# Optimization experiments

Measured on AMD Instinct MI355X. Metric: run time of the kernel, lower is better.

The kernel has to match this reference:

```python
import jax, jax.numpy as jnp
import numpy as np

E, C = 50000, 128  # edges, out_channels (heads=1 so H*C == C)
EPS = 1e-5

def _ln(x, g, b):
    m = x.mean(-1, keepdims=True)
    v = x.var(-1, keepdims=True)
    return (x - m) / jnp.sqrt(v + EPS) * g + b

def _mlp(x, W1, b1, W2, b2):
    return jax.nn.silu(x @ W1 + b1) @ W2 + b2

def setup_inputs() -> dict:
    key = jax.random.key(0)
    ks = jax.random.split(key, 32)
    s = 0.02
    d = {}
    d['edge'] = jax.random.normal(ks[0], (E, C), jnp.float32)
    d['edge_nei_len'] = jax.random.normal(ks[1], (E, 3, C), jnp.float32)
    d['edge_nei_angle'] = jax.random.normal(ks[2], (E, 3, C), jnp.float32)
    # lin_query / lin_key / lin_value (C -> H*C == C)
    d['Wq'] = jax.random.normal(ks[3], (C, C), jnp.float32) * s
    d['bq'] = jnp.zeros((C,), jnp.float32)
    d['Wk'] = jax.random.normal(ks[4], (C, C), jnp.float32) * s
    d['bk'] = jnp.zeros((C,), jnp.float32)
    d['Wv'] = jax.random.normal(ks[5], (C, C), jnp.float32) * s
    d['bv'] = jnp.zeros((C,), jnp.float32)
    # lin_key_e1/e2/e3 and lin_value_e1/e2/e3 stacked along first axis (3 lattice dirs)
    d['Wke'] = jax.random.normal(ks[6], (3, C, C), jnp.float32) * s
    d['bke'] = jnp.zeros((3, C), jnp.float32)
    d['Wve'] = jax.random.normal(ks[7], (3, C, C), jnp.float32) * s
    d['bve'] = jnp.zeros((3, C), jnp.float32)
    # lin_edge (no bias)
    d['We'] = jax.random.normal(ks[8], (C, C), jnp.float32) * s
    # lin_concate
    d['Wc'] = jax.random.normal(ks[9], (C, C), jnp.float32) * s
    d['bc'] = jnp.zeros((C,), jnp.float32)
    # key_update MLP: 3C -> C -> C
    d['Wk1'] = jax.random.normal(ks[10], (3 * C, C), jnp.float32) * s
    d['bk1'] = jnp.zeros((C,), jnp.float32)
    d['Wk2'] = jax.random.normal(ks[11], (C, C), jnp.float32) * s
    d['bk2'] = jnp.zeros((C,), jnp.float32)
    # lin_msg_update MLP: 3C -> C -> C
    d['Wm1'] = jax.random.normal(ks[12], (3 * C, C), jnp.float32) * s
    d['bm1'] = jnp.zeros((C,), jnp.float32)
    d['Wm2'] = jax.random.normal(ks[13], (C, C), jnp.float32) * s
    d['bm2'] = jnp.zeros((C,), jnp.float32)
    # LayerNorms
    d['g_att'] = jnp.ones((C,), jnp.float32)
    d['b_att'] = jnp.zeros((C,), jnp.float32)
    d['g_bn'] = jnp.ones((C,), jnp.float32)
    d['b_bn'] = jnp.zeros((C,), jnp.float32)
    return d

def reference(edge, edge_nei_len, edge_nei_angle,
              Wq, bq, Wk, bk, Wv, bv,
              Wke, bke, Wve, bve, We, Wc, bc,
              Wk1, bk1, Wk2, bk2, Wm1, bm1, Wm2, bm2,
              g_att, b_att, g_bn, b_bn):
    # per-edge projections, broadcast over the 3 lattice directions (repeat in torch)
    q = (edge @ Wq + bq)[:, None, :]           # [E,1,C]
    kx = (edge @ Wk + bk)[:, None, :]          # [E,1,C]
    vx = (edge @ Wv + bv)[:, None, :]          # [E,1,C]
    kx3 = jnp.broadcast_to(kx, (edge.shape[0], 3, kx.shape[-1]))
    vx3 = jnp.broadcast_to(vx, (edge.shape[0], 3, vx.shape[-1]))
    # per-direction projections of lattice embedding (lin_key_e1..3 / lin_value_e1..3)
    ky = jnp.einsum('eti,tio->eto', edge_nei_len, Wke) + bke   # [E,3,C]
    vy = jnp.einsum('eti,tio->eto', edge_nei_len, Wve) + bve   # [E,3,C]
    exy = edge_nei_angle @ We                                   # [E,3,C]
    # key_update MLP and attention score
    k = _mlp(jnp.concatenate([kx3, ky, exy], axis=-1), Wk1, bk1, Wk2, bk2)  # [E,3,C]
    alpha = q * k / jnp.sqrt(jnp.float32(k.shape[-1]))
    # message MLP, sigmoid gate on LayerNorm'd alpha
    msg = _mlp(jnp.concatenate([vx3, vy, exy], axis=-1), Wm1, bm1, Wm2, bm2)
    out = msg * jax.nn.sigmoid(_ln(alpha, g_att, b_att))
    out = out @ Wc + bc        # lin_concate (H*C -> C)
    out = out.sum(axis=1)      # sum over 3 directions -> [E,C]
    return jax.nn.softplus(edge + _ln(out, g_bn, b_bn))
```

## Files before the change

kernel.cpp:

```cpp
#include <hip/hip_runtime.h>

#define E_TOTAL 50000
#define NTILES  3125

#define OFF_WSB 458752ull
#define OFF_Q   524288ull
#define OFF_EK  (OFF_Q  + 12800000ull)
#define OFF_EM  (OFF_EK + 12800000ull)
#define OFF_SK  (OFF_EM + 12800000ull)
#define OFF_SM  (OFF_SK + 38400000ull)
#define WS_NEED (OFF_SM + 38400000ull)

typedef float f4  __attribute__((ext_vector_type(4)));
typedef short s8v __attribute__((ext_vector_type(8)));
typedef short s4v __attribute__((ext_vector_type(4)));

typedef __attribute__((address_space(3))) unsigned lds_u32;
typedef __attribute__((address_space(1))) const unsigned g_u32;

__device__ __forceinline__ short f2bf(float x){
  unsigned u = __builtin_bit_cast(unsigned, x);
  u += 0x7fffu + ((u >> 16) & 1u);
  return (short)(u >> 16);
}
__device__ __forceinline__ float bf2f(short s){
  unsigned u = ((unsigned)(unsigned short)s) << 16;
  return __builtin_bit_cast(float, u);
}
__device__ __forceinline__ float sigm(float x){ return 1.f/(1.f + __expf(-x)); }

__device__ __forceinline__ s8v load_bfrag(const float* p){
  f4 a = *(const f4*)p;
  f4 b = *(const f4*)(p + 4);
  s8v r;
  r[0]=f2bf(a[0]); r[1]=f2bf(a[1]); r[2]=f2bf(a[2]); r[3]=f2bf(a[3]);
  r[4]=f2bf(b[0]); r[5]=f2bf(b[1]); r[6]=f2bf(b[2]); r[7]=f2bf(b[3]);
  return r;
}

__device__ __forceinline__ void mm8l(f4* acc, const s8v* B, const s8v* A, int lane){
  #pragma unroll
  for (int mb = 0; mb < 8; ++mb){
    #pragma unroll
    for (int kk = 0; kk < 4; ++kk){
      s8v af = A[(mb*4 + kk)*64 + lane];
      acc[mb] = __builtin_amdgcn_mfma_f32_16x16x32_bf16(af, B[kk], acc[mb], 0, 0, 0);
    }
  }
}

__device__ __forceinline__ void mm8f(f4* acc, const s8v* B, const s8v* A, int lane){
  #pragma unroll
  for (int mb = 0; mb < 8; mb += 2){
    #pragma unroll
    for (int m2 = 0; m2 < 2; ++m2){
      #pragma unroll
      for (int kk = 0; kk < 4; ++kk){
        s8v af = A[((mb+m2)*4 + kk)*64 + lane];
        acc[mb+m2] = __builtin_amdgcn_mfma_f32_16x16x32_bf16(af, B[kk], acc[mb+m2], 0, 0, 0);
      }
    }
    __builtin_amdgcn_sched_barrier(0);
  }
}

__device__ __forceinline__ void stage_mat(const short* __restrict__ src,
                                          short* dst, int wid, int lane){
  #pragma unroll
  for (int j = 0; j < 8; ++j){
    const short* gsrc = src + j*2048 + wid*512 + lane*8;
    short* ldst = dst + j*2048 + wid*512;
    __builtin_amdgcn_global_load_lds((g_u32*)(const void*)gsrc, (lds_u32*)(void*)ldst, 16, 0, 0);
  }
}

__device__ __forceinline__ s8v pack_pair(const f4& a0, const f4& a1){
  s8v o;
  #pragma unroll
  for (int p = 0; p < 4; ++p){ o[p] = f2bf(a0[p]); o[4+p] = f2bf(a1[p]); }
  return o;
}

__global__ __launch_bounds__(256) void pack_weights(
    const float* __restrict__ Wq, const float* __restrict__ Wk, const float* __restrict__ Wv,
    const float* __restrict__ Wke, const float* __restrict__ Wve, const float* __restrict__ We,
    const float* __restrict__ Wc, const float* __restrict__ Wk1, const float* __restrict__ Wk2,
    const float* __restrict__ Wm1, const float* __restrict__ Wm2,
    short* __restrict__ wsm)
{
  int mi   = blockIdx.x >> 6;
  int elem = ((blockIdx.x & 63) << 8) + threadIdx.x;
  int p  = elem & 7;
  int l  = (elem >> 3) & 63;
  int kk = (elem >> 9) & 3;
  int mb = elem >> 11;
  int gg = l >> 4;
  int m  = mb*16 + (l & 15);
  bool dlay = (mi == 5) || (mi == 6) || (mi == 7);
  int k = dlay ? (kk*32 + ((p < 4) ? (gg*4 + p) : (16 + gg*4 + (p - 4))))
               : (kk*32 + gg*8 + p);

  const float* X = nullptr; const float* Y = nullptr; const float* W = nullptr;
  switch (mi){
    case 0: W = Wq; break;
    case 1: X = Wk; Y = Wk1;            break;
    case 2: X = Wv; Y = Wm1;            break;
    case 3: X = We; Y = Wk1 + 256*128;  break;
    case 4: X = We; Y = Wm1 + 256*128;  break;
    case 5: W = Wk2; break;
    case 6: W = Wm2; break;
    case 7: W = Wc;  break;
    default:
      if (mi < 11){ X = Wke + (mi-8)*16384;  Y = Wk1 + 128*128; }
      else        { X = Wve + (mi-11)*16384; Y = Wm1 + 128*128; }
  }
  float v;
  if (W){
    v = W[k*128 + m];
  } else {
    v = 0.f;
    for (int j = 0; j < 128; ++j) v += X[k*128 + j] * Y[j*128 + m];
  }
  wsm[(size_t)mi*16384 + elem] = f2bf(v);
}

__global__ __launch_bounds__(128) void make_biases(
    const float* __restrict__ bk,  const float* __restrict__ bke, const float* __restrict__ bk1,
    const float* __restrict__ bv,  const float* __restrict__ bve, const float* __restrict__ bm1,
    const float* __restrict__ Wk1, const float* __restrict__ Wm1,
    float* __restrict__ wsb)
{
  int b = blockIdx.x;
  int t = b % 3;
  bool isM = b >= 3;
  int o = threadIdx.x;
  const float* W  = isM ? Wm1 : Wk1;
  const float* b0 = isM ? bv  : bk;
  const float* be = (isM ? bve : bke) + t*128;
  const float* b1 = isM ? bm1 : bk1;
  float v = b1[o];
  for (int j = 0; j < 128; ++j)
    v += b0[j]*W[j*128 + o] + be[j]*W[(128 + j)*128 + o];
  wsb[b*128 + o] = v;
}

__global__ __launch_bounds__(256) void proj(
    const float* __restrict__ edge, const float* __restrict__ bq,
    const short* __restrict__ wsm, char* __restrict__ ws)
{
  __shared__ short lds[3*16384];
  const int lane = threadIdx.x & 63;
  const int wid  = threadIdx.x >> 6;
  stage_mat(wsm + 0*16384, lds,          wid, lane);
  stage_mat(wsm + 1*16384, lds + 16384,  wid, lane);
  stage_mat(wsm + 2*16384, lds + 32768,  wid, lane);
  __syncthreads();
  const int g = lane >> 4, er = lane & 15;
  short* wq  = (short*)(ws + OFF_Q);
  short* wek = (short*)(ws + OFF_EK);
  short* wem = (short*)(ws + OFF_EM);

  #pragma unroll 1
  for (int tile = blockIdx.x*4 + wid; tile < NTILES; tile += 1024){
    const float* erow = edge + ((size_t)tile*16 + er)*128;
    s8v BE[4];
    #pragma unroll
    for (int kk = 0; kk < 4; ++kk) BE[kk] = load_bfrag(erow + kk*32 + g*8);

    f4 acc[8];
    #pragma unroll
    for (int mb = 0; mb < 8; ++mb) acc[mb] = *(const f4*)(bq + mb*16 + g*4);
    mm8f(acc, BE, (const s8v*)lds, lane);
    #pragma unroll
    for (int c = 0; c < 4; ++c)
      *(s8v*)(wq + (size_t)tile*2048 + c*512 + lane*8) = pack_pair(acc[2*c], acc[2*c+1]);

    #pragma unroll
    for (int mb = 0; mb < 8; ++mb){ f4 z = {0.f,0.f,0.f,0.f}; acc[mb] = z; }
    mm8f(acc, BE, (const s8v*)(lds + 16384), lane);
    #pragma unroll
    for (int c = 0; c < 4; ++c)
      *(s8v*)(wek + (size_t)tile*2048 + c*512 + lane*8) = pack_pair(acc[2*c], acc[2*c+1]);

    #pragma unroll
    for (int mb = 0; mb < 8; ++mb){ f4 z = {0.f,0.f,0.f,0.f}; acc[mb] = z; }
    mm8f(acc, BE, (const s8v*)(lds + 32768), lane);
    #pragma unroll
    for (int c = 0; c < 4; ++c)
      *(s8v*)(wem + (size_t)tile*2048 + c*512 + lane*8) = pack_pair(acc[2*c], acc[2*c+1]);
  }
}

__global__ __launch_bounds__(256) void hpass(
    const float* __restrict__ nlen, const float* __restrict__ nang,
    const short* __restrict__ wsm, const float* __restrict__ wsb,
    char* __restrict__ ws)
{
  __shared__ short lds[4*16384];
  const int lane = threadIdx.x & 63;
  const int wid  = threadIdx.x >> 6;
  const int t    = blockIdx.y;
  stage_mat(wsm + (size_t)(8 + t)*16384,  lds,         wid, lane);
  stage_mat(wsm + 3*16384,                lds + 16384, wid, lane);
  stage_mat(wsm + (size_t)(11 + t)*16384, lds + 32768, wid, lane);
  stage_mat(wsm + 4*16384,                lds + 49152, wid, lane);
  __syncthreads();
  const int g = lane >> 4, er = lane & 15;
  const float* biasK = wsb + t*128;
  const float* biasM = wsb + 384 + t*128;
  const short* wek = (const short*)(ws + OFF_EK);
  const short* wem = (const short*)(ws + OFF_EM);
  short* wsk  = (short*)(ws + OFF_SK + (size_t)t*12800000ull);
  short* wsm2 = (short*)(ws + OFF_SM + (size_t)t*12800000ull);

  #pragma unroll 1
  for (int tile = blockIdx.x*4 + wid; tile < NTILES; tile += 340){
    const size_t e = (size_t)tile*16 + er;
    const float* lrow = nlen + (e*3 + t)*128;
    const float* arow = nang + (e*3 + t)*128;
    s8v BL[4], BA[4];
    #pragma unroll
    for (int kk = 0; kk < 4; ++kk){
      BL[kk] = load_bfrag(lrow + kk*32 + g*8);
      BA[kk] = load_bfrag(arow + kk*32 + g*8);
    }
    f4 acc[8];
    #pragma unroll
    for (int c = 0; c < 4; ++c){
      s8v ek8 = *(const s8v*)(wek + (size_t)tile*2048 + c*512 + lane*8);
      f4 b0 = *(const f4*)(biasK + (2*c)*16 + g*4);
      f4 b1 = *(const f4*)(biasK + (2*c+1)*16 + g*4);
      #pragma unroll
      for (int r = 0; r < 4; ++r){ b0[r] += bf2f(ek8[r]); b1[r] += bf2f(ek8[4+r]); }
      acc[2*c] = b0; acc[2*c+1] = b1;
    }
    mm8f(acc, BL, (const s8v*)lds, lane);
    mm8f(acc, BA, (const s8v*)(lds + 16384), lane);
    #pragma unroll
    for (int kk = 0; kk < 4; ++kk){
      s8v S;
      #pragma unroll
      for (int p = 0; p < 4; ++p){
        float x0 = acc[2*kk][p];   S[p]   = f2bf(x0 * sigm(x0));
        float x1 = acc[2*kk+1][p]; S[4+p] = f2bf(x1 * sigm(x1));
      }
      *(s8v*)(wsk + (size_t)tile*2048 + kk*512 + lane*8) = S;
    }
    #pragma unroll
    for (int c = 0; c < 4; ++c){
      s8v em8 = *(const s8v*)(wem + (size_t)tile*2048 + c*512 + lane*8);
      f4 b0 = *(const f4*)(biasM + (2*c)*16 + g*4);
      f4 b1 = *(const f4*)(biasM + (2*c+1)*16 + g*4);
      #pragma unroll
      for (int r = 0; r < 4; ++r){ b0[r] += bf2f(em8[r]); b1[r] += bf2f(em8[4+r]); }
      acc[2*c] = b0; acc[2*c+1] = b1;
    }
    mm8f(acc, BL, (const s8v*)(lds + 32768), lane);
    mm8f(acc, BA, (const s8v*)(lds + 49152), lane);
    #pragma unroll
    for (int kk = 0; kk < 4; ++kk){
      s8v S;
      #pragma unroll
      for (int p = 0; p < 4; ++p){
        float x0 = acc[2*kk][p];   S[p]   = f2bf(x0 * sigm(x0));
        float x1 = acc[2*kk+1][p]; S[4+p] = f2bf(x1 * sigm(x1));
      }
      *(s8v*)(wsm2 + (size_t)tile*2048 + kk*512 + lane*8) = S;
    }
  }
}

__global__ __launch_bounds__(256) void gfin(
    const float* __restrict__ edge,
    const float* __restrict__ bk2,  const float* __restrict__ bm2,
    const float* __restrict__ bc,
    const float* __restrict__ g_att, const float* __restrict__ b_att,
    const float* __restrict__ g_bn,  const float* __restrict__ b_bn,
    const short* __restrict__ wsm, const char* __restrict__ ws,
    float* __restrict__ out)
{
  __shared__ short lds[3*16384];
  const int lane = threadIdx.x & 63;
  const int wid  = threadIdx.x >> 6;
  stage_mat(wsm + 5*16384, lds,         wid, lane);
  stage_mat(wsm + 6*16384, lds + 16384, wid, lane);
  stage_mat(wsm + 7*16384, lds + 32768, wid, lane);
  __syncthreads();
  const int g = lane >> 4, er = lane & 15;
  const short* wq = (const short*)(ws + OFF_Q);

  #pragma unroll 1
  for (int tile = blockIdx.x*4 + wid; tile < NTILES; tile += 1024){
    const size_t e = (size_t)tile*16 + er;
    f4 gm[8], acc[8], gate[8];
    #pragma unroll
    for (int mb = 0; mb < 8; ++mb){ f4 z = {0.f,0.f,0.f,0.f}; gm[mb] = z; }

    #pragma unroll 1
    for (int t = 0; t < 3; ++t){
      const short* wsk  = (const short*)(ws + OFF_SK + (size_t)t*12800000ull);
      const short* wsm2 = (const short*)(ws + OFF_SM + (size_t)t*12800000ull);
      s8v SF[4];
      #pragma unroll
      for (int kk = 0; kk < 4; ++kk)
        SF[kk] = *(const s8v*)(wsk + (size_t)tile*2048 + kk*512 + lane*8);
      #pragma unroll
      for (int mb = 0; mb < 8; ++mb) acc[mb] = *(const f4*)(bk2 + mb*16 + g*4);
      mm8f(acc, SF, (const s8v*)lds, lane);

      float sm = 0.f, ssq = 0.f;
      #pragma unroll
      for (int c = 0; c < 4; ++c){
        s8v q8 = *(const s8v*)(wq + (size_t)tile*2048 + c*512 + lane*8);
        #pragma unroll
        for (int r = 0; r < 4; ++r){
          float a = bf2f(q8[r])   * acc[2*c][r]   * 0.08838834764831845f;
          float b = bf2f(q8[4+r]) * acc[2*c+1][r] * 0.08838834764831845f;
          acc[2*c][r] = a; acc[2*c+1][r] = b;
          sm += a + b; ssq += a*a + b*b;
        }
      }
      sm  += __shfl_xor(sm, 16);  sm  += __shfl_xor(sm, 32);
      ssq += __shfl_xor(ssq, 16); ssq += __shfl_xor(ssq, 32);
      float mean = sm * (1.f/128.f);
      float rstd = rsqrtf(ssq * (1.f/128.f) - mean*mean + 1e-5f);
      #pragma unroll
      for (int mb = 0; mb < 8; ++mb){
        f4 ga = *(const f4*)(g_att + mb*16 + g*4);
        f4 bb = *(const f4*)(b_att + mb*16 + g*4);
        #pragma unroll
        for (int r = 0; r < 4; ++r)
          gate[mb][r] = sigm((acc[mb][r] - mean)*rstd*ga[r] + bb[r]);
      }

      #pragma unroll
      for (int kk = 0; kk < 4; ++kk)
        SF[kk] = *(const s8v*)(wsm2 + (size_t)tile*2048 + kk*512 + lane*8);
      #pragma unroll
      for (int mb = 0; mb < 8; ++mb) acc[mb] = *(const f4*)(bm2 + mb*16 + g*4);
      mm8f(acc, SF, (const s8v*)(lds + 16384), lane);
      #pragma unroll
      for (int mb = 0; mb < 8; ++mb){
        #pragma unroll
        for (int r = 0; r < 4; ++r) gm[mb][r] += acc[mb][r] * gate[mb][r];
      }
    }

    s8v GF[4];
    #pragma unroll
    for (int c = 0; c < 4; ++c) GF[c] = pack_pair(gm[2*c], gm[2*c+1]);
    #pragma unroll
    for (int mb = 0; mb < 8; ++mb){
      f4 b = *(const f4*)(bc + mb*16 + g*4);
      #pragma unroll
      for (int r = 0; r < 4; ++r) b[r] *= 3.f;
      acc[mb] = b;
    }
    mm8f(acc, GF, (const s8v*)(lds + 32768), lane);

    float sm = 0.f, ssq = 0.f;
    #pragma unroll
    for (int mb = 0; mb < 8; ++mb){
      #pragma unroll
      for (int r = 0; r < 4; ++r){ sm += acc[mb][r]; ssq += acc[mb][r]*acc[mb][r]; }
    }
    sm  += __shfl_xor(sm, 16);  sm  += __shfl_xor(sm, 32);
    ssq += __shfl_xor(ssq, 16); ssq += __shfl_xor(ssq, 32);
    float mean = sm * (1.f/128.f);
    float rstd = rsqrtf(ssq * (1.f/128.f) - mean*mean + 1e-5f);

    const float* erow = edge + e*128;
    #pragma unroll
    for (int mb = 0; mb < 8; ++mb){
      f4 ev  = *(const f4*)(erow + mb*16 + g*4);
      f4 gv  = *(const f4*)(g_bn + mb*16 + g*4);
      f4 bv2 = *(const f4*)(b_bn + mb*16 + g*4);
      f4 o;
      #pragma unroll
      for (int r = 0; r < 4; ++r){
        float x = ev[r] + (acc[mb][r] - mean)*rstd*gv[r] + bv2[r];
        o[r] = (x > 20.f) ? x : __logf(1.f + __expf(x));
      }
      *(f4*)(out + e*128 + mb*16 + g*4) = o;
    }
  }
}

__global__ __launch_bounds__(256) void edge_fused(
    const float* __restrict__ edge, const float* __restrict__ nlen, const float* __restrict__ nang,
    const float* __restrict__ bq,   const float* __restrict__ bk2,  const float* __restrict__ bm2,
    const float* __restrict__ bc,
    const float* __restrict__ g_att, const float* __restrict__ b_att,
    const float* __restrict__ g_bn,  const float* __restrict__ b_bn,
    const short* __restrict__ wsm,  const float* __restrict__ wsb,
    float* __restrict__ out)
{
  __shared__ short smem[2*16384];
  const int lane = threadIdx.x & 63;
  const int wid  = threadIdx.x >> 6;
  int tile = blockIdx.x*4 + wid;
  if (tile > NTILES-1) tile = NTILES-1;
  const int g  = lane >> 4;
  const int er = lane & 15;
  const size_t e = (size_t)tile*16 + er;
  const float* erow = edge + e*128;

  stage_mat(wsm + 0*16384, smem, wid, lane);
  s8v BE[4];
  #pragma unroll
  for (int kk = 0; kk < 4; ++kk) BE[kk] = load_bfrag(erow + kk*32 + g*8);
  f4 acc[8], gm[8];
  s4v qb[8], ekb[8], emb[8], gateb[8];
  s8v S[4], BL[4], BA[4];
  #pragma unroll
  for (int mb = 0; mb < 8; ++mb){ f4 z = {0.f,0.f,0.f,0.f}; gm[mb] = z; }
  __syncthreads();

  stage_mat(wsm + 1*16384, smem + 16384, wid, lane);
  #pragma unroll
  for (int mb = 0; mb < 8; ++mb) acc[mb] = *(const f4*)(bq + mb*16 + g*4);
  mm8l(acc, BE, (const s8v*)smem, lane);
  #pragma unroll
  for (int mb = 0; mb < 8; ++mb){
    s4v t4; t4[0]=f2bf(acc[mb][0]); t4[1]=f2bf(acc[mb][1]); t4[2]=f2bf(acc[mb][2]); t4[3]=f2bf(acc[mb][3]);
    qb[mb] = t4;
  }
  __syncthreads();

  stage_mat(wsm + 2*16384, smem, wid, lane);
  #pragma unroll
  for (int mb = 0; mb < 8; ++mb){ f4 z = {0.f,0.f,0.f,0.f}; acc[mb] = z; }
  mm8l(acc, BE, (const s8v*)(smem + 16384), lane);
  #pragma unroll
  for (int mb = 0; mb < 8; ++mb){
    s4v t4; t4[0]=f2bf(acc[mb][0]); t4[1]=f2bf(acc[mb][1]); t4[2]=f2bf(acc[mb][2]); t4[3]=f2bf(acc[mb][3]);
    ekb[mb] = t4;
  }
  __syncthreads();

  stage_mat(wsm + 8*16384, smem + 16384, wid, lane);
  #pragma unroll
  for (int mb = 0; mb < 8; ++mb){ f4 z = {0.f,0.f,0.f,0.f}; acc[mb] = z; }
  mm8l(acc, BE, (const s8v*)smem, lane);
  #pragma unroll
  for (int mb = 0; mb < 8; ++mb){
    s4v t4; t4[0]=f2bf(acc[mb][0]); t4[1]=f2bf(acc[mb][1]); t4[2]=f2bf(acc[mb][2]); t4[3]=f2bf(acc[mb][3]);
    emb[mb] = t4;
  }
  {
    const float* lrow = nlen + e*3*128;
    const float* arow = nang + e*3*128;
    #pragma unroll
    for (int kk = 0; kk < 4; ++kk){
      BL[kk] = load_bfrag(lrow + kk*32 + g*8);
      BA[kk] = load_bfrag(arow + kk*32 + g*8);
    }
  }
  __syncthreads();

  int cur = 1;
  #pragma unroll 1
  for (int t = 0; t < 3; ++t){
    stage_mat(wsm + 3*16384, smem + (cur^1)*16384, wid, lane);
    #pragma unroll
    for (int mb = 0; mb < 8; ++mb){
      f4 b = *(const f4*)(wsb + t*128 + mb*16 + g*4);
      #pragma unroll
      for (int r = 0; r < 4; ++r) b[r] += bf2f(ekb[mb][r]);
      acc[mb] = b;
    }
    mm8l(acc, BL, (const s8v*)(smem + cur*16384), lane);
    __syncthreads(); cur ^= 1;

    stage_mat(wsm + 5*16384, smem + (cur^1)*16384, wid, lane);
    mm8l(acc, BA, (const s8v*)(smem + cur*16384), lane);
    #pragma unroll
    for (int kk = 0; kk < 4; ++kk){
      #pragma unroll
      for (int p = 0; p < 4; ++p){
        float x0 = acc[2*kk][p];   S[kk][p]   = f2bf(x0 * sigm(x0));
        float x1 = acc[2*kk+1][p]; S[kk][4+p] = f2bf(x1 * sigm(x1));
      }
    }
    __syncthreads(); cur ^= 1;

    stage_mat(wsm + (size_t)(11+t)*16384, smem + (cur^1)*16384, wid, lane);
    #pragma unroll
    for (int mb = 0; mb < 8; ++mb) acc[mb] = *(const f4*)(bk2 + mb*16 + g*4);
    mm8l(acc, S, (const s8v*)(smem + cur*16384), lane);
    {
      float sm = 0.f, ssq = 0.f;
      #pragma unroll
      for (int mb = 0; mb < 8; ++mb){
        #pragma unroll
        for (int r = 0; r < 4; ++r){
          float a = bf2f(qb[mb][r]) * acc[mb][r] * 0.08838834764831845f;
          acc[mb][r] = a; sm += a; ssq += a*a;
        }
      }
      sm  += __shfl_xor(sm, 16);  sm  += __shfl_xor(sm, 32);
      ssq += __shfl_xor(ssq, 16); ssq += __shfl_xor(ssq, 32);
      float mean = sm * (1.f/128.f);
      float rstd = rsqrtf(ssq * (1.f/128.f) - mean*mean + 1e-5f);
      #pragma unroll
      for (int mb = 0; mb < 8; ++mb){
        f4 ga = *(const f4*)(g_att + mb*16 + g*4);
        f4 bb = *(const f4*)(b_att + mb*16 + g*4);
        s4v t4;
        #pragma unroll
        for (int r = 0; r < 4; ++r)
          t4[r] = f2bf(sigm((acc[mb][r] - mean)*rstd*ga[r] + bb[r]));
        gateb[mb] = t4;
      }
    }
    __syncthreads(); cur ^= 1;

    stage_mat(wsm + 4*16384, smem + (cur^1)*16384, wid, lane);
    #pragma unroll
    for (int mb = 0; mb < 8; ++mb){
      f4 b = *(const f4*)(wsb + 384 + t*128 + mb*16 + g*4);
      #pragma unroll
      for (int r = 0; r < 4; ++r) b[r] += bf2f(emb[mb][r]);
      acc[mb] = b;
    }
    mm8l(acc, BL, (const s8v*)(smem + cur*16384), lane);
    __syncthreads(); cur ^= 1;

    stage_mat(wsm + 6*16384, smem + (cur^1)*16384, wid, lane);
    mm8l(acc, BA, (const s8v*)(smem + cur*16384), lane);
    #pragma unroll
    for (int kk = 0; kk < 4; ++kk){
      #pragma unroll
      for (int p = 0; p < 4; ++p){
        float x0 = acc[2*kk][p];   S[kk][p]   = f2bf(x0 * sigm(x0));
        float x1 = acc[2*kk+1][p]; S[kk][4+p] = f2bf(x1 * sigm(x1));
      }
    }
    __syncthreads(); cur ^= 1;

    stage_mat(wsm + (size_t)(t < 2 ? 9 + t : 7)*16384, smem + (cur^1)*16384, wid, lane);
    #pragma unroll
    for (int mb = 0; mb < 8; ++mb) acc[mb] = *(const f4*)(bm2 + mb*16 + g*4);
    mm8l(acc, S, (const s8v*)(smem + cur*16384), lane);
    if (t < 2){
      const float* lrow = nlen + (e*3 + t + 1)*128;
      const float* arow = nang + (e*3 + t + 1)*128;
      #pragma unroll
      for (int kk = 0; kk < 4; ++kk){
        BL[kk] = load_bfrag(lrow + kk*32 + g*8);
        BA[kk] = load_bfrag(arow + kk*32 + g*8);
      }
    }
    #pragma unroll
    for (int mb = 0; mb < 8; ++mb){
      #pragma unroll
      for (int r = 0; r < 4; ++r) gm[mb][r] += acc[mb][r] * bf2f(gateb[mb][r]);
    }
    __syncthreads(); cur ^= 1;
  }

  s8v GF[4];
  #pragma unroll
  for (int kk = 0; kk < 4; ++kk){
    #pragma unroll
    for (int p = 0; p < 4; ++p){
      GF[kk][p]   = f2bf(gm[2*kk][p]);
      GF[kk][4+p] = f2bf(gm[2*kk+1][p]);
    }
  }
  #pragma unroll
  for (int mb = 0; mb < 8; ++mb){
    f4 b = *(const f4*)(bc + mb*16 + g*4);
    #pragma unroll
    for (int r = 0; r < 4; ++r) b[r] *= 3.f;
    acc[mb] = b;
  }
  mm8l(acc, GF, (const s8v*)(smem + cur*16384), lane);

  float sm = 0.f, ssq = 0.f;
  #pragma unroll
  for (int mb = 0; mb < 8; ++mb){
    #pragma unroll
    for (int r = 0; r < 4; ++r){ sm += acc[mb][r]; ssq += acc[mb][r]*acc[mb][r]; }
  }
  sm  += __shfl_xor(sm, 16);  sm  += __shfl_xor(sm, 32);
  ssq += __shfl_xor(ssq, 16); ssq += __shfl_xor(ssq, 32);
  float mean = sm * (1.f/128.f);
  float rstd = rsqrtf(ssq * (1.f/128.f) - mean*mean + 1e-5f);

  #pragma unroll
  for (int mb = 0; mb < 8; ++mb){
    f4 ev  = *(const f4*)(erow + mb*16 + g*4);
    f4 gv  = *(const f4*)(g_bn + mb*16 + g*4);
    f4 bv2 = *(const f4*)(b_bn + mb*16 + g*4);
    f4 o;
    #pragma unroll
    for (int r = 0; r < 4; ++r){
      float x = ev[r] + (acc[mb][r] - mean)*rstd*gv[r] + bv2[r];
      o[r] = (x > 20.f) ? x : log1pf(__expf(x));
    }
    *(f4*)(out + e*128 + mb*16 + g*4) = o;
  }
}

extern "C" void kernel_launch(void* const* d_in, const int* in_sizes, int n_in,
                              void* d_out, int out_size, void* d_ws, size_t ws_size,
                              hipStream_t stream)
{
  const float* edge = (const float*)d_in[0];
  const float* nlen = (const float*)d_in[1];
  const float* nang = (const float*)d_in[2];
  const float* Wq  = (const float*)d_in[3];
  const float* bq  = (const float*)d_in[4];
  const float* Wk  = (const float*)d_in[5];
  const float* bk  = (const float*)d_in[6];
  const float* Wv  = (const float*)d_in[7];
  const float* bv  = (const float*)d_in[8];
  const float* Wke = (const float*)d_in[9];
  const float* bke = (const float*)d_in[10];
  const float* Wve = (const float*)d_in[11];
  const float* bve = (const float*)d_in[12];
  const float* We  = (const float*)d_in[13];
  const float* Wc  = (const float*)d_in[14];
  const float* bc  = (const float*)d_in[15];
  const float* Wk1 = (const float*)d_in[16];
  const float* bk1 = (const float*)d_in[17];
  const float* Wk2 = (const float*)d_in[18];
  const float* bk2 = (const float*)d_in[19];
  const float* Wm1 = (const float*)d_in[20];
  const float* bm1 = (const float*)d_in[21];
  const float* Wm2 = (const float*)d_in[22];
  const float* bm2 = (const float*)d_in[23];
  const float* g_att = (const float*)d_in[24];
  const float* b_att = (const float*)d_in[25];
  const float* g_bn  = (const float*)d_in[26];
  const float* b_bn  = (const float*)d_in[27];

  short* wsm = (short*)d_ws;
  float* wsb = (float*)((char*)d_ws + OFF_WSB);
  char*  ws  = (char*)d_ws;

  pack_weights<<<dim3(14*64), dim3(256), 0, stream>>>(
      Wq, Wk, Wv, Wke, Wve, We, Wc, Wk1, Wk2, Wm1, Wm2, wsm);
  make_biases<<<dim3(6), dim3(128), 0, stream>>>(
      bk, bke, bk1, bv, bve, bm1, Wk1, Wm1, wsb);

  if (ws_size >= WS_NEED){
    proj<<<dim3(256), dim3(256), 0, stream>>>(edge, bq, wsm, ws);
    hpass<<<dim3(85, 3), dim3(256), 0, stream>>>(nlen, nang, wsm, wsb, ws);
    gfin<<<dim3(256), dim3(256), 0, stream>>>(
        edge, bk2, bm2, bc, g_att, b_att, g_bn, b_bn, wsm, ws, (float*)d_out);
  } else {
    edge_fused<<<dim3((NTILES + 3)/4), dim3(256), 0, stream>>>(
        edge, nlen, nang, bq, bk2, bm2, bc, g_att, b_att, g_bn, b_bn,
        wsm, wsb, (float*)d_out);
  }
}
```

Baseline: 179.6 us.

## Split hidden-layer pass into separate key and message kernels with halved LDS

The hidden-layer pass that computed both the key-MLP and message-MLP first layers is split into two kernels, each staging only two weight matrices (64 KB LDS instead of 128 KB) and launched with twice as many blocks. Bias vectors are hoisted into registers before the tile loop. The aim is higher occupancy and more parallelism per kernel, at the cost of reading the neighbor length/angle inputs twice from global memory and an extra kernel launch.

```diff
diff --git a/kernel.cpp b/kernel.cpp
--- a/kernel.cpp
+++ b/kernel.cpp
@@ -191,30 +191,28 @@
   }
 }
 
-__global__ __launch_bounds__(256) void hpass(
+__global__ __launch_bounds__(256) void hpassK(
     const float* __restrict__ nlen, const float* __restrict__ nang,
     const short* __restrict__ wsm, const float* __restrict__ wsb,
     char* __restrict__ ws)
 {
-  __shared__ short lds[4*16384];
+  __shared__ short lds[2*16384];
   const int lane = threadIdx.x & 63;
   const int wid  = threadIdx.x >> 6;
   const int t    = blockIdx.y;
-  stage_mat(wsm + (size_t)(8 + t)*16384,  lds,         wid, lane);
-  stage_mat(wsm + 3*16384,                lds + 16384, wid, lane);
-  stage_mat(wsm + (size_t)(11 + t)*16384, lds + 32768, wid, lane);
-  stage_mat(wsm + 4*16384,                lds + 49152, wid, lane);
+  stage_mat(wsm + (size_t)(8 + t)*16384, lds,         wid, lane);
+  stage_mat(wsm + 3*16384,               lds + 16384, wid, lane);
   __syncthreads();
   const int g = lane >> 4, er = lane & 15;
-  const float* biasK = wsb + t*128;
-  const float* biasM = wsb + 384 + t*128;
   const short* wek = (const short*)(ws + OFF_EK);
-  const short* wem = (const short*)(ws + OFF_EM);
-  short* wsk  = (short*)(ws + OFF_SK + (size_t)t*12800000ull);
-  short* wsm2 = (short*)(ws + OFF_SM + (size_t)t*12800000ull);
+  short* wsk = (short*)(ws + OFF_SK + (size_t)t*12800000ull);
+
+  f4 bK[8];
+  #pragma unroll
+  for (int mb = 0; mb < 8; ++mb) bK[mb] = *(const f4*)(wsb + t*128 + mb*16 + g*4);
 
   #pragma unroll 1
-  for (int tile = blockIdx.x*4 + wid; tile < NTILES; tile += 340){
+  for (int tile = blockIdx.x*4 + wid; tile < NTILES; tile += 680){
     const size_t e = (size_t)tile*16 + er;
     const float* lrow = nlen + (e*3 + t)*128;
     const float* arow = nang + (e*3 + t)*128;
@@ -228,8 +226,7 @@
     #pragma unroll
     for (int c = 0; c < 4; ++c){
       s8v ek8 = *(const s8v*)(wek + (size_t)tile*2048 + c*512 + lane*8);
-      f4 b0 = *(const f4*)(biasK + (2*c)*16 + g*4);
-      f4 b1 = *(const f4*)(biasK + (2*c+1)*16 + g*4);
+      f4 b0 = bK[2*c], b1 = bK[2*c+1];
       #pragma unroll
       for (int r = 0; r < 4; ++r){ b0[r] += bf2f(ek8[r]); b1[r] += bf2f(ek8[4+r]); }
       acc[2*c] = b0; acc[2*c+1] = b1;
@@ -246,17 +243,51 @@
       }
       *(s8v*)(wsk + (size_t)tile*2048 + kk*512 + lane*8) = S;
     }
+  }
+}
+
+__global__ __launch_bounds__(256) void hpassM(
+    const float* __restrict__ nlen, const float* __restrict__ nang,
+    const short* __restrict__ wsm, const float* __restrict__ wsb,
+    char* __restrict__ ws)
+{
+  __shared__ short lds[2*16384];
+  const int lane = threadIdx.x & 63;
+  const int wid  = threadIdx.x >> 6;
+  const int t    = blockIdx.y;
+  stage_mat(wsm + (size_t)(11 + t)*16384, lds,         wid, lane);
+  stage_mat(wsm + 4*16384,                lds + 16384, wid, lane);
+  __syncthreads();
+  const int g = lane >> 4, er = lane & 15;
+  const short* wem = (const short*)(ws + OFF_EM);
+  short* wsm2 = (short*)(ws + OFF_SM + (size_t)t*12800000ull);
+
+  f4 bM[8];
+  #pragma unroll
+  for (int mb = 0; mb < 8; ++mb) bM[mb] = *(const f4*)(wsb + 384 + t*128 + mb*16 + g*4);
+
+  #pragma unroll 1
+  for (int tile = blockIdx.x*4 + wid; tile < NTILES; tile += 680){
+    const size_t e = (size_t)tile*16 + er;
+    const float* lrow = nlen + (e*3 + t)*128;
+    const float* arow = nang + (e*3 + t)*128;
+    s8v BL[4], BA[4];
+    #pragma unroll
+    for (int kk = 0; kk < 4; ++kk){
+      BL[kk] = load_bfrag(lrow + kk*32 + g*8);
+      BA[kk] = load_bfrag(arow + kk*32 + g*8);
+    }
+    f4 acc[8];
     #pragma unroll
     for (int c = 0; c < 4; ++c){
       s8v em8 = *(const s8v*)(wem + (size_t)tile*2048 + c*512 + lane*8);
-      f4 b0 = *(const f4*)(biasM + (2*c)*16 + g*4);
-      f4 b1 = *(const f4*)(biasM + (2*c+1)*16 + g*4);
+      f4 b0 = bM[2*c], b1 = bM[2*c+1];
       #pragma unroll
       for (int r = 0; r < 4; ++r){ b0[r] += bf2f(em8[r]); b1[r] += bf2f(em8[4+r]); }
       acc[2*c] = b0; acc[2*c+1] = b1;
     }
-    mm8f(acc, BL, (const s8v*)(lds + 32768), lane);
-    mm8f(acc, BA, (const s8v*)(lds + 49152), lane);
+    mm8f(acc, BL, (const s8v*)lds, lane);
+    mm8f(acc, BA, (const s8v*)(lds + 16384), lane);
     #pragma unroll
     for (int kk = 0; kk < 4; ++kk){
       s8v S;
@@ -647,7 +678,8 @@
 
   if (ws_size >= WS_NEED){
     proj<<<dim3(256), dim3(256), 0, stream>>>(edge, bq, wsm, ws);
-    hpass<<<dim3(85, 3), dim3(256), 0, stream>>>(nlen, nang, wsm, wsb, ws);
+    hpassK<<<dim3(170, 3), dim3(256), 0, stream>>>(nlen, nang, wsm, wsb, ws);
+    hpassM<<<dim3(170, 3), dim3(256), 0, stream>>>(nlen, nang, wsm, wsb, ws);
     gfin<<<dim3(256), dim3(256), 0, stream>>>(
         edge, bk2, bm2, bc, g_att, b_att, g_bn, b_bn, wsm, ws, (float*)d_out);
   } else {
```

Measured after the change: 203.0 us. 1.13x slower.

## Split hidden-layer pass into separate key and message blocks to halve LDS

Applied to the files above, without the earlier changes.

The hidden-layer kernel used to compute both the key-MLP and message-MLP first layers in one block, holding four weight matrices in LDS. It now launches a third grid dimension that picks key or message, so each block stages only two matrices and each doubled-grid block does one branch. Bias fragments are also hoisted into registers before the loop. Halving LDS per block should let more blocks share a CU. The cost is that each block reads nlen and nang again, so the global traffic for those inputs doubles.

```diff
diff --git a/kernel.cpp b/kernel.cpp
--- a/kernel.cpp
+++ b/kernel.cpp
@@ -191,30 +191,30 @@
   }
 }
 
-__global__ __launch_bounds__(256) void hpass(
+__global__ __launch_bounds__(256) void hsplit(
     const float* __restrict__ nlen, const float* __restrict__ nang,
     const short* __restrict__ wsm, const float* __restrict__ wsb,
     char* __restrict__ ws)
 {
-  __shared__ short lds[4*16384];
+  __shared__ short lds[2*16384];
   const int lane = threadIdx.x & 63;
   const int wid  = threadIdx.x >> 6;
   const int t    = blockIdx.y;
-  stage_mat(wsm + (size_t)(8 + t)*16384,  lds,         wid, lane);
-  stage_mat(wsm + 3*16384,                lds + 16384, wid, lane);
-  stage_mat(wsm + (size_t)(11 + t)*16384, lds + 32768, wid, lane);
-  stage_mat(wsm + 4*16384,                lds + 49152, wid, lane);
+  const int isM  = blockIdx.z;
+  stage_mat(wsm + (size_t)(isM ? 11 + t : 8 + t)*16384, lds,         wid, lane);
+  stage_mat(wsm + (size_t)(isM ? 4 : 3)*16384,          lds + 16384, wid, lane);
   __syncthreads();
   const int g = lane >> 4, er = lane & 15;
-  const float* biasK = wsb + t*128;
-  const float* biasM = wsb + 384 + t*128;
-  const short* wek = (const short*)(ws + OFF_EK);
-  const short* wem = (const short*)(ws + OFF_EM);
-  short* wsk  = (short*)(ws + OFF_SK + (size_t)t*12800000ull);
-  short* wsm2 = (short*)(ws + OFF_SM + (size_t)t*12800000ull);
+  const short* win = (const short*)(ws + (isM ? OFF_EM : OFF_EK));
+  short* wout = (short*)(ws + (isM ? OFF_SM : OFF_SK) + (size_t)t*12800000ull);
+  const float* bsrc = wsb + (isM ? 384 : 0) + t*128;
+
+  f4 bias[8];
+  #pragma unroll
+  for (int mb = 0; mb < 8; ++mb) bias[mb] = *(const f4*)(bsrc + mb*16 + g*4);
 
   #pragma unroll 1
-  for (int tile = blockIdx.x*4 + wid; tile < NTILES; tile += 340){
+  for (int tile = blockIdx.x*4 + wid; tile < NTILES; tile += 680){
     const size_t e = (size_t)tile*16 + er;
     const float* lrow = nlen + (e*3 + t)*128;
     const float* arow = nang + (e*3 + t)*128;
@@ -227,11 +227,10 @@
     f4 acc[8];
     #pragma unroll
     for (int c = 0; c < 4; ++c){
-      s8v ek8 = *(const s8v*)(wek + (size_t)tile*2048 + c*512 + lane*8);
-      f4 b0 = *(const f4*)(biasK + (2*c)*16 + g*4);
-      f4 b1 = *(const f4*)(biasK + (2*c+1)*16 + g*4);
-      #pragma unroll
-      for (int r = 0; r < 4; ++r){ b0[r] += bf2f(ek8[r]); b1[r] += bf2f(ek8[4+r]); }
+      s8v x8 = *(const s8v*)(win + (size_t)tile*2048 + c*512 + lane*8);
+      f4 b0 = bias[2*c], b1 = bias[2*c+1];
+      #pragma unroll
+      for (int r = 0; r < 4; ++r){ b0[r] += bf2f(x8[r]); b1[r] += bf2f(x8[4+r]); }
       acc[2*c] = b0; acc[2*c+1] = b1;
     }
     mm8f(acc, BL, (const s8v*)lds, lane);
@@ -244,28 +243,7 @@
         float x0 = acc[2*kk][p];   S[p]   = f2bf(x0 * sigm(x0));
         float x1 = acc[2*kk+1][p]; S[4+p] = f2bf(x1 * sigm(x1));
       }
-      *(s8v*)(wsk + (size_t)tile*2048 + kk*512 + lane*8) = S;
-    }
-    #pragma unroll
-    for (int c = 0; c < 4; ++c){
-      s8v em8 = *(const s8v*)(wem + (size_t)tile*2048 + c*512 + lane*8);
-      f4 b0 = *(const f4*)(biasM + (2*c)*16 + g*4);
-      f4 b1 = *(const f4*)(biasM + (2*c+1)*16 + g*4);
-      #pragma unroll
-      for (int r = 0; r < 4; ++r){ b0[r] += bf2f(em8[r]); b1[r] += bf2f(em8[4+r]); }
-      acc[2*c] = b0; acc[2*c+1] = b1;
-    }
-    mm8f(acc, BL, (const s8v*)(lds + 32768), lane);
-    mm8f(acc, BA, (const s8v*)(lds + 49152), lane);
-    #pragma unroll
-    for (int kk = 0; kk < 4; ++kk){
-      s8v S;
-      #pragma unroll
-      for (int p = 0; p < 4; ++p){
-        float x0 = acc[2*kk][p];   S[p]   = f2bf(x0 * sigm(x0));
-        float x1 = acc[2*kk+1][p]; S[4+p] = f2bf(x1 * sigm(x1));
-      }
-      *(s8v*)(wsm2 + (size_t)tile*2048 + kk*512 + lane*8) = S;
+      *(s8v*)(wout + (size_t)tile*2048 + kk*512 + lane*8) = S;
     }
   }
 }
@@ -647,7 +625,7 @@
 
   if (ws_size >= WS_NEED){
     proj<<<dim3(256), dim3(256), 0, stream>>>(edge, bq, wsm, ws);
-    hpass<<<dim3(85, 3), dim3(256), 0, stream>>>(nlen, nang, wsm, wsb, ws);
+    hsplit<<<dim3(170, 3, 2), dim3(256), 0, stream>>>(nlen, nang, wsm, wsb, ws);
     gfin<<<dim3(256), dim3(256), 0, stream>>>(
         edge, bk2, bm2, bc, g_att, b_att, g_bn, b_bn, wsm, ws, (float*)d_out);
   } else {
```

After: 195.6 us. +8.9%, slower.
